# Kernel optimization log

Hardware: AMD Instinct MI355X
Metric: run time of the kernel (lower is better)

The kernel has to match this reference:

```python
import jax, jax.numpy as jnp
import numpy as np
from jax import lax

D_MODEL, D_INNER, D_STATE, D_CONV, DT_RANK = 1024, 2048, 16, 4, 64
B, L = 1, 2048


def setup_inputs() -> dict:
    key = jax.random.key(0)
    ks = jax.random.split(key, 10)
    s = lambda d: 1.0 / np.sqrt(d)
    return {
        "x": jax.random.normal(ks[0], (B, L, D_MODEL), jnp.float32),
        "W_in": jax.random.normal(ks[1], (D_MODEL, 2 * D_INNER), jnp.float32) * s(D_MODEL),
        "conv_w": jax.random.normal(ks[2], (D_INNER, D_CONV), jnp.float32) * s(D_CONV),
        "conv_b": jax.random.normal(ks[3], (D_INNER,), jnp.float32) * 0.01,
        "W_x": jax.random.normal(ks[4], (D_INNER, DT_RANK + 2 * D_STATE), jnp.float32) * s(D_INNER),
        "W_dt": jax.random.normal(ks[5], (DT_RANK, D_INNER), jnp.float32) * s(DT_RANK),
        "b_dt": jax.random.normal(ks[6], (D_INNER,), jnp.float32) * 0.01,
        # A = arange(1, d_state+1) repeated over d_inner; A_log = log(A)
        "A_log": jnp.log(jnp.tile(jnp.arange(1.0, D_STATE + 1.0, dtype=jnp.float32), (D_INNER, 1))),
        "D": jnp.ones((D_INNER,), jnp.float32),
        "W_out": jax.random.normal(ks[7], (D_INNER, D_MODEL), jnp.float32) * s(D_INNER),
    }


def reference(x, W_in, conv_w, conv_b, W_x, W_dt, b_dt, A_log, D, W_out):
    b, l, dm = x.shape
    di, n = A_log.shape[0], A_log.shape[1]
    # input projection + split into conv branch and gate residual
    x_and_res = x @ W_in                          # (b, l, 2*di)
    xc, res = x_and_res[..., :di], x_and_res[..., di:]
    # causal depthwise conv1d (left pad k-1, matches torch padding=k-1 + slice[:l])
    k = conv_w.shape[1]
    xp = jnp.pad(xc, ((0, 0), (k - 1, 0), (0, 0)))
    xconv = conv_b
    for j in range(k):
        xconv = xconv + xp[:, j:j + l, :] * conv_w[:, j]
    xs = jax.nn.silu(xconv)                       # (b, l, di)
    # selection parameters
    x_dbl = xs @ W_x                              # (b, l, dt_rank + 2n)
    dt_r = x_dbl[..., :DT_RANK]
    Bm = x_dbl[..., DT_RANK:DT_RANK + n]          # (b, l, n)
    Cm = x_dbl[..., DT_RANK + n:]                 # (b, l, n)
    dt = jax.nn.softplus(dt_r @ W_dt + b_dt)      # (b, l, di)
    A = -jnp.exp(A_log)                           # (di, n)
    # discretize
    dA = jnp.exp(jnp.einsum('bld,dn->bldn', dt, A))
    dBx = jnp.einsum('bld,bln->bldn', dt, Bm) * xs[..., None]
    # sequential state scan over time
    def step(h, inp):
        dA_t, dBx_t, C_t = inp                    # (b,di,n),(b,di,n),(b,n)
        h = dA_t * h + dBx_t
        y = jnp.einsum('bdn,bn->bd', h, C_t)
        return h, y
    h0 = jnp.zeros((b, di, n), x.dtype)
    hT, ys = lax.scan(step, h0, (dA.transpose(1, 0, 2, 3),
                                 dBx.transpose(1, 0, 2, 3),
                                 Cm.transpose(1, 0, 2)))
    y = ys.transpose(1, 0, 2) + xs * D            # (b, l, di)
    y = y * jax.nn.silu(res)
    out = y @ W_out                               # (b, l, d_model)
    return out, hT
```

## Files before the change

### kernel.cpp

```cpp
#include <hip/hip_runtime.h>
#include <math.h>

#define DM 1024
#define DI 2048
#define NS 16
#define DTR 64
#define LL 2048
#define NXDBL 96
#define NCHUNK 128
#define CHLEN 16

typedef unsigned short u16;
typedef __attribute__((ext_vector_type(8))) short short8;
typedef __attribute__((ext_vector_type(8))) unsigned short us8;
typedef __attribute__((ext_vector_type(4))) float f32x4;

__device__ __forceinline__ float sigmoidf_(float x) { return 1.f / (1.f + __expf(-x)); }
__device__ __forceinline__ float siluf_(float x) { return x * sigmoidf_(x); }
__device__ __forceinline__ float softplus_fast(float x) {
    return fmaxf(x, 0.f) + __logf(1.f + __expf(-fabsf(x)));
}
__device__ __forceinline__ u16 f2b(float f) {
    unsigned u = __float_as_uint(f);
    return (u16)((u + 0x7FFFu + ((u >> 16) & 1u)) >> 16);
}
__device__ __forceinline__ float b2f(u16 h) {
    return __uint_as_float(((unsigned)h) << 16);
}
__device__ __forceinline__ unsigned pack2(float lo, float hi) {
    return (unsigned)f2b(lo) | ((unsigned)f2b(hi) << 16);
}

__device__ __forceinline__ void convT_dev(const float* __restrict__ src,
                                          u16* __restrict__ dst, int R, int C,
                                          int bflat, int gridx, float (*t)[33]) {
    const int tx = threadIdx.x & 31, ty = threadIdx.x >> 5;
    const int c0 = (bflat % gridx) * 32, r0 = (bflat / gridx) * 32;
#pragma unroll
    for (int i = 0; i < 4; i++)
        t[ty + i * 8][tx] = src[(size_t)(r0 + ty + i * 8) * C + c0 + tx];
    __syncthreads();
#pragma unroll
    for (int i = 0; i < 4; i++)
        dst[(size_t)(c0 + ty + i * 8) * R + r0 + tx] = f2b(t[tx][ty + i * 8]);
}

#define PREP_BLOCKS 8640
__global__ __launch_bounds__(256) void prep_all(const float* __restrict__ x,
                                                u16* __restrict__ xb,
                                                const float* __restrict__ W_in,
                                                u16* __restrict__ W_inT,
                                                const float* __restrict__ W_out,
                                                u16* __restrict__ W_outT,
                                                const float* __restrict__ W_x,
                                                u16* __restrict__ W_xT_pad) {
    __shared__ float t[32][33];
    const int b = blockIdx.x;
    if (b < 2048) {
        const int i = (b * 256 + threadIdx.x) * 4;
        float4 v = *(const float4*)&x[i];
        u16 o[4] = {f2b(v.x), f2b(v.y), f2b(v.z), f2b(v.w)};
        *(ushort4*)&xb[i] = *(ushort4*)o;
    } else if (b < 6144) {
        convT_dev(W_in, W_inT, DM, 2 * DI, b - 2048, 2 * DI / 32, t);
    } else if (b < 8192) {
        convT_dev(W_out, W_outT, DI, DM, b - 6144, DM / 32, t);
    } else if (b < 8384) {
        convT_dev(W_x, W_xT_pad, DI, NXDBL, b - 8192, NXDBL / 32, t);
    } else {
        const int i = (b - 8384) * 256 + threadIdx.x;
        if (i < 32 * DI) W_xT_pad[96 * DI + i] = 0;
    }
}

#define WAITV(N) asm volatile("s_waitcnt vmcnt(" #N ")" ::: "memory")
template <int EPI, int NSTEPS>
__global__ __launch_bounds__(256) void gemm_mfma(const u16* __restrict__ A,
                                                 const u16* __restrict__ Bt,
                                                 void* __restrict__ C0,
                                                 void* __restrict__ C1,
                                                 int M, int N, int lda, int nreal) {
    __shared__ u16 As[3][128 * 32];
    __shared__ u16 Bs[3][128 * 32];
    const int tid = threadIdx.x;
    const int lane = tid & 63;
    const int wave = tid >> 6;
    const int gx = gridDim.x, gy = gridDim.y;
    const int nb = gx * gy;
    const int h = blockIdx.y * gx + blockIdx.x;
    const int f = (h & 7) * (nb >> 3) + (h >> 3);
    const int bm = (f % gy) * 128, bn = (f / gy) * 128;
    const int wr = wave >> 1, wc = wave & 1;
    const int k_off = blockIdx.z * (NSTEPS * 32);

    f32x4 acc[4][4];
#pragma unroll
    for (int m = 0; m < 4; m++)
#pragma unroll
        for (int n = 0; n < 4; n++) acc[m][n] = (f32x4)0.f;

    const int srow = tid >> 2;
    const int swz = (tid >> 3) & 3;
    const int skel = (((tid & 3) ^ swz) << 3);
    const u16* Ag0 = A + (size_t)(bm + srow) * lda + k_off + skel;
    const u16* Ag1 = A + (size_t)(bm + 64 + srow) * lda + k_off + skel;
    const u16* Bg0 = Bt + (size_t)(bn + srow) * lda + k_off + skel;
    const u16* Bg1 = Bt + (size_t)(bn + 64 + srow) * lda + k_off + skel;
    u16* Asl = &As[0][0] + tid * 8;
    u16* Bsl = &Bs[0][0] + tid * 8;

    const int rsw = (lane >> 1) & 3;
    const int arow = (wr * 64 + (lane & 15)) * 32 + (((lane >> 4) ^ rsw) << 3);
    const int brow = (wc * 64 + (lane & 15)) * 32 + (((lane >> 4) ^ rsw) << 3);

#define STAGE(buf, ks)                                                               \
    do {                                                                             \
        __builtin_amdgcn_global_load_lds(                                            \
            (const __attribute__((address_space(1))) unsigned*)(Ag0 + (ks)),         \
            (__attribute__((address_space(3))) unsigned*)(Asl + (buf) * 4096),       \
            16, 0, 0);                                                               \
        __builtin_amdgcn_global_load_lds(                                            \
            (const __attribute__((address_space(1))) unsigned*)(Ag1 + (ks)),         \
            (__attribute__((address_space(3))) unsigned*)(Asl + (buf) * 4096 + 2048),\
            16, 0, 0);                                                               \
        __builtin_amdgcn_global_load_lds(                                            \
            (const __attribute__((address_space(1))) unsigned*)(Bg0 + (ks)),         \
            (__attribute__((address_space(3))) unsigned*)(Bsl + (buf) * 4096),       \
            16, 0, 0);                                                               \
        __builtin_amdgcn_global_load_lds(                                            \
            (const __attribute__((address_space(1))) unsigned*)(Bg1 + (ks)),         \
            (__attribute__((address_space(3))) unsigned*)(Bsl + (buf) * 4096 + 2048),\
            16, 0, 0);                                                               \
    } while (0)

#define COMPUTE(buf)                                                                 \
    do {                                                                             \
        short8 av[4], bv[4];                                                         \
        _Pragma("unroll") for (int m = 0; m < 4; m++)                                \
            av[m] = *(const short8*)&As[buf][arow + m * 512];                        \
        _Pragma("unroll") for (int n = 0; n < 4; n++)                                \
            bv[n] = *(const short8*)&Bs[buf][brow + n * 512];                        \
        _Pragma("unroll") for (int m = 0; m < 4; m++)                                \
            _Pragma("unroll") for (int n = 0; n < 4; n++)                            \
                acc[m][n] = __builtin_amdgcn_mfma_f32_16x16x32_bf16(av[m], bv[n],    \
                                                                    acc[m][n], 0, 0, 0); \
    } while (0)

    STAGE(0, 0);
    if (NSTEPS > 1) STAGE(1, 32);
#pragma unroll
    for (int s = 0; s < NSTEPS; ++s) {
        if (s + 2 < NSTEPS) {
            STAGE((s + 2) % 3, (s + 2) * 32);
            WAITV(8);
        } else if (s + 1 < NSTEPS) {
            WAITV(4);
        } else {
            WAITV(0);
        }
        __builtin_amdgcn_s_barrier();
        COMPUTE(s % 3);
        __builtin_amdgcn_s_barrier();
    }
#undef STAGE
#undef COMPUTE

    const int crow0 = bm + wr * 64 + (lane >> 4) * 4;
    const int ccol0 = bn + wc * 64 + (lane & 15);
#pragma unroll
    for (int m = 0; m < 4; m++)
#pragma unroll
        for (int n = 0; n < 4; n++) {
            const int col = ccol0 + n * 16;
#pragma unroll
            for (int r = 0; r < 4; r++) {
                const int row = crow0 + m * 16 + r;
                const float v = acc[m][n][r];
                if (EPI == 1) {
                    if (col < DI)
                        ((u16*)C0)[(size_t)row * DI + col] = f2b(v);
                    else
                        ((u16*)C1)[(size_t)row * DI + col - DI] = f2b(siluf_(v));
                } else if (EPI == 2) {
                    u16* C0z = (u16*)C0 + (size_t)blockIdx.z * M * nreal;
                    if (col < nreal) C0z[(size_t)row * nreal + col] = f2b(v);
                } else {
                    float* C0z = (float*)C0 + (size_t)blockIdx.z * M * nreal;
                    if (col < nreal) C0z[(size_t)row * nreal + col] = v;
                }
            }
        }
}

__global__ __launch_bounds__(256) void gemm128_dt(const float* __restrict__ A,
                                                  const float* __restrict__ B,
                                                  const float* __restrict__ bias,
                                                  const u16* __restrict__ xsb,
                                                  unsigned* __restrict__ dtxs,
                                                  int N, int K, int lda) {
    __shared__ float As[16][132];
    __shared__ float Bs[16][132];
    const int tid = threadIdx.x;
    const int bm = blockIdx.y * 128, bn = blockIdx.x * 128;
    const int ty = tid >> 4, tx = tid & 15;
    float acc[8][8];
#pragma unroll
    for (int i = 0; i < 8; i++)
#pragma unroll
        for (int j = 0; j < 8; j++) acc[i][j] = 0.f;

    const int ar = tid >> 2, ak = (tid & 3) << 2;
    const int bk = tid >> 5, bc = (tid & 31) << 2;

    for (int k0 = 0; k0 < K; k0 += 16) {
        float4 a0 = *(const float4*)&A[(size_t)(bm + ar) * lda + k0 + ak];
        float4 a1 = *(const float4*)&A[(size_t)(bm + ar + 64) * lda + k0 + ak];
        float4 b0 = *(const float4*)&B[(size_t)(k0 + bk) * N + bn + bc];
        float4 b1 = *(const float4*)&B[(size_t)(k0 + bk + 8) * N + bn + bc];
        __syncthreads();
        As[ak + 0][ar] = a0.x; As[ak + 1][ar] = a0.y;
        As[ak + 2][ar] = a0.z; As[ak + 3][ar] = a0.w;
        As[ak + 0][ar + 64] = a1.x; As[ak + 1][ar + 64] = a1.y;
        As[ak + 2][ar + 64] = a1.z; As[ak + 3][ar + 64] = a1.w;
        *(float4*)&Bs[bk][bc] = b0;
        *(float4*)&Bs[bk + 8][bc] = b1;
        __syncthreads();
#pragma unroll
        for (int k = 0; k < 16; k++) {
            float a[8], b[8];
            *(float4*)&a[0] = *(const float4*)&As[k][ty * 8];
            *(float4*)&a[4] = *(const float4*)&As[k][ty * 8 + 4];
            *(float4*)&b[0] = *(const float4*)&Bs[k][tx * 8];
            *(float4*)&b[4] = *(const float4*)&Bs[k][tx * 8 + 4];
#pragma unroll
            for (int i = 0; i < 8; i++)
#pragma unroll
                for (int j = 0; j < 8; j++) acc[i][j] = fmaf(a[i], b[j], acc[i][j]);
        }
    }
#pragma unroll
    for (int i = 0; i < 8; i++) {
        const int row = bm + ty * 8 + i;
#pragma unroll
        for (int j = 0; j < 8; j += 4) {
            const int col = bn + tx * 8 + j;
            const float4 bi = *(const float4*)&bias[col];
            ushort4 xv = *(const ushort4*)&xsb[(size_t)row * N + col];
            unsigned o[4];
            o[0] = (unsigned)f2b(softplus_fast(acc[i][j + 0] + bi.x)) |
                   ((unsigned)xv.x << 16);
            o[1] = (unsigned)f2b(softplus_fast(acc[i][j + 1] + bi.y)) |
                   ((unsigned)xv.y << 16);
            o[2] = (unsigned)f2b(softplus_fast(acc[i][j + 2] + bi.z)) |
                   ((unsigned)xv.z << 16);
            o[3] = (unsigned)f2b(softplus_fast(acc[i][j + 3] + bi.w)) |
                   ((unsigned)xv.w << 16);
            *(uint4*)&dtxs[(size_t)row * N + col] = *(uint4*)o;
        }
    }
}

__global__ __launch_bounds__(256) void sum4b(const u16* __restrict__ p,
                                             float* __restrict__ out, int n) {
    const int i = (blockIdx.x * 256 + threadIdx.x) * 8;
    us8 a = *(const us8*)&p[i];
    us8 b = *(const us8*)&p[(size_t)n + i];
    us8 c = *(const us8*)&p[2 * (size_t)n + i];
    us8 d = *(const us8*)&p[3 * (size_t)n + i];
    float o[8];
#pragma unroll
    for (int q = 0; q < 8; q++)
        o[q] = (b2f(a[q]) + b2f(b[q])) + (b2f(c[q]) + b2f(d[q]));
    *(float4*)&out[i] = *(float4*)&o[0];
    *(float4*)&out[i + 4] = *(float4*)&o[4];
}

__global__ __launch_bounds__(256) void g2reduce(const float* __restrict__ part,
                                                float* __restrict__ xdbl) {
    const int gid = blockIdx.x * 256 + threadIdx.x;
    if (gid < LL * NXDBL) {
        float s = 0.f;
#pragma unroll
        for (int z = 0; z < 16; z++) s += part[(size_t)z * LL * NXDBL + gid];
        xdbl[gid] = s;
    }
}

__global__ __launch_bounds__(256) void conv_silu(const u16* __restrict__ xcb,
                                                 const float* __restrict__ cw,
                                                 const float* __restrict__ cb,
                                                 u16* __restrict__ xsb) {
    const int gid = (blockIdx.x * 256 + threadIdx.x) * 4;
    const int l = gid >> 11;
    const int d = gid & (DI - 1);
    float acc[4];
    {
        float4 b4 = *(const float4*)&cb[d];
        acc[0] = b4.x; acc[1] = b4.y; acc[2] = b4.z; acc[3] = b4.w;
    }
    float4 w0 = *(const float4*)&cw[(d + 0) * 4];
    float4 w1 = *(const float4*)&cw[(d + 1) * 4];
    float4 w2 = *(const float4*)&cw[(d + 2) * 4];
    float4 w3 = *(const float4*)&cw[(d + 3) * 4];
    const float* wp0 = (const float*)&w0;
    const float* wp1 = (const float*)&w1;
    const float* wp2 = (const float*)&w2;
    const float* wp3 = (const float*)&w3;
#pragma unroll
    for (int j = 0; j < 4; j++) {
        const int li = l + j - 3;
        if (li >= 0) {
            ushort4 v = *(const ushort4*)&xcb[(size_t)li * DI + d];
            acc[0] = fmaf(b2f(v.x), wp0[j], acc[0]);
            acc[1] = fmaf(b2f(v.y), wp1[j], acc[1]);
            acc[2] = fmaf(b2f(v.z), wp2[j], acc[2]);
            acc[3] = fmaf(b2f(v.w), wp3[j], acc[3]);
        }
    }
    u16 ob[4] = {f2b(siluf_(acc[0])), f2b(siluf_(acc[1])),
                 f2b(siluf_(acc[2])), f2b(siluf_(acc[3]))};
    *(ushort4*)&xsb[gid] = *(ushort4*)ob;
}

__global__ __launch_bounds__(256) void scan_phase1(const unsigned* __restrict__ dtxs,
                                                   const float* __restrict__ xdbl,
                                                   const float* __restrict__ A_log,
                                                   u16* __restrict__ chA,
                                                   u16* __restrict__ chB) {
    const int g = blockIdx.x * 256 + threadIdx.x;
    const int d = g & (DI - 1);
    const int c = g >> 11;
    float An2[NS], ap[NS], bc[NS];
    {
        float al[NS];
#pragma unroll
        for (int q = 0; q < 4; q++)
            *(float4*)&al[q * 4] = *(const float4*)&A_log[d * NS + q * 4];
#pragma unroll
        for (int n = 0; n < NS; n++) {
            An2[n] = -__expf(al[n]) * 1.44269504f;
            ap[n] = 1.f;
            bc[n] = 0.f;
        }
    }
    const int l0 = c * CHLEN;
    for (int l = l0; l < l0 + CHLEN; ++l) {
        const unsigned dx2 = dtxs[(size_t)l * DI + d];
        const float dtv = b2f((u16)(dx2 & 0xffff));
        const float xsv = b2f((u16)(dx2 >> 16));
        const float dx = dtv * xsv;
        float bv[NS];
#pragma unroll
        for (int q = 0; q < 4; q++)
            *(float4*)&bv[q * 4] = *(const float4*)&xdbl[(size_t)l * NXDBL + DTR + q * 4];
#pragma unroll
        for (int n = 0; n < NS; n++) {
            const float al = __builtin_amdgcn_exp2f(dtv * An2[n]);
            ap[n] *= al;
            bc[n] = fmaf(al, bc[n], dx * bv[n]);
        }
    }
    const size_t o = ((size_t)c * DI + d) * NS;
    u16 ta[NS], tb[NS];
#pragma unroll
    for (int n = 0; n < NS; n++) { ta[n] = f2b(ap[n]); tb[n] = f2b(bc[n]); }
    *(us8*)&chA[o] = *(us8*)&ta[0];
    *(us8*)&chA[o + 8] = *(us8*)&ta[8];
    *(us8*)&chB[o] = *(us8*)&tb[0];
    *(us8*)&chB[o + 8] = *(us8*)&tb[8];
}

__global__ __launch_bounds__(256) void scan_phase2(u16* __restrict__ chA,
                                                   const u16* __restrict__ chB,
                                                   float* __restrict__ hT_out) {
    const int p = blockIdx.x * 256 + threadIdx.x;
    const size_t base = (size_t)2 * p;
    float h0f = 0.f, h1f = 0.f;
#pragma unroll 16
    for (int c = 0; c < NCHUNK; ++c) {
        const size_t o = (size_t)c * DI * NS + base;
        const unsigned av = *(const unsigned*)&chA[o];
        const unsigned bv = *(const unsigned*)&chB[o];
        *(unsigned*)&chA[o] = pack2(h0f, h1f);
        h0f = fmaf(b2f((u16)(av & 0xffff)), h0f, b2f((u16)(bv & 0xffff)));
        h1f = fmaf(b2f((u16)(av >> 16)), h1f, b2f((u16)(bv >> 16)));
    }
    *(float2*)&hT_out[base] = make_float2(h0f, h1f);
}

__global__ __launch_bounds__(256) void scan_phase3(const unsigned* __restrict__ dtxs,
                                                   const float* __restrict__ xdbl,
                                                   const float* __restrict__ A_log,
                                                   const u16* __restrict__ h0,
                                                   const float* __restrict__ Dw,
                                                   const u16* __restrict__ gate,
                                                   u16* __restrict__ yb) {
    const int g = blockIdx.x * 256 + threadIdx.x;
    const int d = g & (DI - 1);
    const int c = g >> 11;
    float An2[NS], h[NS];
    {
        float al[NS];
#pragma unroll
        for (int q = 0; q < 4; q++)
            *(float4*)&al[q * 4] = *(const float4*)&A_log[d * NS + q * 4];
#pragma unroll
        for (int n = 0; n < NS; n++) An2[n] = -__expf(al[n]) * 1.44269504f;
    }
    {
        const size_t ho = ((size_t)c * DI + d) * NS;
        us8 h0a = *(const us8*)&h0[ho];
        us8 h0b = *(const us8*)&h0[ho + 8];
#pragma unroll
        for (int q = 0; q < 8; q++) {
            h[q] = b2f((u16)h0a[q]);
            h[8 + q] = b2f((u16)h0b[q]);
        }
    }
    const float Dd = Dw[d];
    const int l0 = c * CHLEN;
    for (int l = l0; l < l0 + CHLEN; ++l) {
        const unsigned dx2 = dtxs[(size_t)l * DI + d];
        const float dtv = b2f((u16)(dx2 & 0xffff));
        const float xsv = b2f((u16)(dx2 >> 16));
        const float gv = b2f(gate[(size_t)l * DI + d]);
        const float dx = dtv * xsv;
        float bv[NS], cv[NS];
#pragma unroll
        for (int q = 0; q < 4; q++) {
            *(float4*)&bv[q * 4] = *(const float4*)&xdbl[(size_t)l * NXDBL + DTR + q * 4];
            *(float4*)&cv[q * 4] =
                *(const float4*)&xdbl[(size_t)l * NXDBL + DTR + NS + q * 4];
        }
#pragma unroll
        for (int n = 0; n < NS; n++) {
            const float al = __builtin_amdgcn_exp2f(dtv * An2[n]);
            h[n] = fmaf(al, h[n], dx * bv[n]);
        }
        float y0 = 0.f, y1 = 0.f, y2 = 0.f, y3 = 0.f;
#pragma unroll
        for (int n = 0; n < NS; n += 4) {
            y0 = fmaf(h[n + 0], cv[n + 0], y0);
            y1 = fmaf(h[n + 1], cv[n + 1], y1);
            y2 = fmaf(h[n + 2], cv[n + 2], y2);
            y3 = fmaf(h[n + 3], cv[n + 3], y3);
        }
        const float yv = (((y0 + y1) + (y2 + y3)) + xsv * Dd) * gv;
        yb[(size_t)l * DI + d] = f2b(yv);
    }
}

extern "C" void kernel_launch(void* const* d_in, const int* in_sizes, int n_in,
                              void* d_out, int out_size, void* d_ws, size_t ws_size,
                              hipStream_t stream) {
    const float* x = (const float*)d_in[0];
    const float* W_in = (const float*)d_in[1];
    const float* conv_w = (const float*)d_in[2];
    const float* conv_b = (const float*)d_in[3];
    const float* W_x = (const float*)d_in[4];
    const float* W_dt = (const float*)d_in[5];
    const float* b_dt = (const float*)d_in[6];
    const float* A_log = (const float*)d_in[7];
    const float* Dw = (const float*)d_in[8];
    const float* W_out = (const float*)d_in[9];
    float* out = (float*)d_out;

    float* ws = (float*)d_ws;
    u16*      xcb      = (u16*)ws;
    u16*      gate     = (u16*)(ws + 4194304);
    unsigned* dtxs     = (unsigned*)(ws + 8388608);
    float*    xdbl     = ws + 16777216;
    u16*      chA      = (u16*)(ws + 16973824);
    u16*      chB      = (u16*)(ws + 21168128);
    u16*      xb       = (u16*)(ws + 25362432);
    u16*      W_inT_b  = (u16*)(ws + 26411008);
    u16*      W_outT_b = (u16*)(ws + 28508160);
    u16*      xs_b     = (u16*)(ws + 29556736);
    u16*      W_xT_pad = (u16*)(ws + 31653888);
    float*    g2part   = ws + 31784960;
    u16*      g4part   = (u16*)(ws + 35979264);
    u16*      yb       = (u16*)(ws + 44367872);

    prep_all<<<PREP_BLOCKS, 256, 0, stream>>>(x, xb, W_in, W_inT_b, W_out, W_outT_b,
                                              W_x, W_xT_pad);
    gemm_mfma<1, DM / 32><<<dim3(2 * DI / 128, LL / 128), 256, 0, stream>>>(
        xb, W_inT_b, xcb, gate, LL, 2 * DI, DM, 2 * DI);
    conv_silu<<<(LL * DI) / 1024, 256, 0, stream>>>(xcb, conv_w, conv_b, xs_b);
    gemm_mfma<0, 4><<<dim3(1, LL / 128, 16), 256, 0, stream>>>(
        xs_b, W_xT_pad, g2part, nullptr, LL, 128, DI, NXDBL);
    g2reduce<<<(LL * NXDBL + 255) / 256, 256, 0, stream>>>(g2part, xdbl);
    gemm128_dt<<<dim3(DI / 128, LL / 128), 256, 0, stream>>>(xdbl, W_dt, b_dt, xs_b,
                                                             dtxs, DI, DTR, NXDBL);
    scan_phase1<<<(DI * NCHUNK) / 256, 256, 0, stream>>>(dtxs, xdbl, A_log, chA, chB);
    scan_phase2<<<(DI * NS / 2) / 256, 256, 0, stream>>>(chA, chB,
                                                         out + (size_t)LL * DM);
    scan_phase3<<<(DI * NCHUNK) / 256, 256, 0, stream>>>(dtxs, xdbl, A_log, chA, Dw,
                                                         gate, yb);
    gemm_mfma<2, DI / 128><<<dim3(DM / 128, LL / 128, 4), 256, 0, stream>>>(
        yb, W_outT_b, g4part, nullptr, LL, DM, DI, DM);
    sum4b<<<(LL * DM) / 2048, 256, 0, stream>>>(g4part, out, LL * DM);
}
```

Measured before the change: 164.7 us.

## Split chunk-carry scan into two-level super-chunk scan and widen conv_silu vectors

The serial 128-step carry scan across chunks (phase2, only 64 blocks) becomes two levels. A parallel pass composes 8 sub-chunks per super-chunk and writes exclusive local prefixes back into chA/chB. A short 16-step pass then propagates carries across super-chunks, and phase3 rebuilds each chunk's start state from the super-carry plus the local prefix. The aim is to cut the long dependent latency chain and raise parallelism, at the cost of an extra launch and more memory traffic. conv_silu also processes 8 channels per thread with 16-byte loads and stores instead of 4.

```diff
diff --git a/kernel.cpp b/kernel.cpp
--- a/kernel.cpp
+++ b/kernel.cpp
@@ -9,6 +9,8 @@
 #define NXDBL 96
 #define NCHUNK 128
 #define CHLEN 16
+#define NSUPER 16
+#define SUBCH 8
 
 typedef unsigned short u16;
 typedef __attribute__((ext_vector_type(8))) short short8;
@@ -290,36 +292,36 @@
                                                  const float* __restrict__ cw,
                                                  const float* __restrict__ cb,
                                                  u16* __restrict__ xsb) {
-    const int gid = (blockIdx.x * 256 + threadIdx.x) * 4;
+    const int gid = (blockIdx.x * 256 + threadIdx.x) * 8;
     const int l = gid >> 11;
     const int d = gid & (DI - 1);
-    float acc[4];
+    float acc[8];
     {
-        float4 b4 = *(const float4*)&cb[d];
-        acc[0] = b4.x; acc[1] = b4.y; acc[2] = b4.z; acc[3] = b4.w;
-    }
-    float4 w0 = *(const float4*)&cw[(d + 0) * 4];
-    float4 w1 = *(const float4*)&cw[(d + 1) * 4];
-    float4 w2 = *(const float4*)&cw[(d + 2) * 4];
-    float4 w3 = *(const float4*)&cw[(d + 3) * 4];
-    const float* wp0 = (const float*)&w0;
-    const float* wp1 = (const float*)&w1;
-    const float* wp2 = (const float*)&w2;
-    const float* wp3 = (const float*)&w3;
+        float4 b0 = *(const float4*)&cb[d];
+        float4 b1 = *(const float4*)&cb[d + 4];
+        acc[0] = b0.x; acc[1] = b0.y; acc[2] = b0.z; acc[3] = b0.w;
+        acc[4] = b1.x; acc[5] = b1.y; acc[6] = b1.z; acc[7] = b1.w;
+    }
+    float4 w[8];
+#pragma unroll
+    for (int q = 0; q < 8; q++) w[q] = *(const float4*)&cw[(d + q) * 4];
 #pragma unroll
     for (int j = 0; j < 4; j++) {
         const int li = l + j - 3;
         if (li >= 0) {
-            ushort4 v = *(const ushort4*)&xcb[(size_t)li * DI + d];
-            acc[0] = fmaf(b2f(v.x), wp0[j], acc[0]);
-            acc[1] = fmaf(b2f(v.y), wp1[j], acc[1]);
-            acc[2] = fmaf(b2f(v.z), wp2[j], acc[2]);
-            acc[3] = fmaf(b2f(v.w), wp3[j], acc[3]);
-        }
-    }
-    u16 ob[4] = {f2b(siluf_(acc[0])), f2b(siluf_(acc[1])),
-                 f2b(siluf_(acc[2])), f2b(siluf_(acc[3]))};
-    *(ushort4*)&xsb[gid] = *(ushort4*)ob;
+            us8 v = *(const us8*)&xcb[(size_t)li * DI + d];
+            const float wj0[8] = {((const float*)&w[0])[j], ((const float*)&w[1])[j],
+                                  ((const float*)&w[2])[j], ((const float*)&w[3])[j],
+                                  ((const float*)&w[4])[j], ((const float*)&w[5])[j],
+                                  ((const float*)&w[6])[j], ((const float*)&w[7])[j]};
+#pragma unroll
+            for (int q = 0; q < 8; q++) acc[q] = fmaf(b2f(v[q]), wj0[q], acc[q]);
+        }
+    }
+    u16 ob[8];
+#pragma unroll
+    for (int q = 0; q < 8; q++) ob[q] = f2b(siluf_(acc[q]));
+    *(us8*)&xsb[gid] = *(us8*)ob;
 }
 
 __global__ __launch_bounds__(256) void scan_phase1(const unsigned* __restrict__ dtxs,
@@ -370,20 +372,48 @@
     *(us8*)&chB[o + 8] = *(us8*)&tb[8];
 }
 
-__global__ __launch_bounds__(256) void scan_phase2(u16* __restrict__ chA,
-                                                   const u16* __restrict__ chB,
-                                                   float* __restrict__ hT_out) {
+__global__ __launch_bounds__(256) void scan_phase2a(u16* __restrict__ chA,
+                                                    u16* __restrict__ chB,
+                                                    float* __restrict__ supA,
+                                                    float* __restrict__ supB) {
+    const int G = blockIdx.x * 256 + threadIdx.x;
+    const int s = G >> 14;
+    const int p = G & 16383;
+    const size_t base = (size_t)2 * p;
+    float af0 = 1.f, bf0 = 0.f, af1 = 1.f, bf1 = 0.f;
+#pragma unroll
+    for (int k = 0; k < SUBCH; ++k) {
+        const int c = s * SUBCH + k;
+        const size_t o = (size_t)c * DI * NS + base;
+        const unsigned av = *(const unsigned*)&chA[o];
+        const unsigned bvv = *(const unsigned*)&chB[o];
+        *(unsigned*)&chA[o] = pack2(af0, af1);
+        *(unsigned*)&chB[o] = pack2(bf0, bf1);
+        const float a0 = b2f((u16)(av & 0xffff)), a1 = b2f((u16)(av >> 16));
+        const float b0 = b2f((u16)(bvv & 0xffff)), b1 = b2f((u16)(bvv >> 16));
+        bf0 = fmaf(a0, bf0, b0); af0 *= a0;
+        bf1 = fmaf(a1, bf1, b1); af1 *= a1;
+    }
+    const size_t so = (size_t)s * (DI * NS) + base;
+    *(float2*)&supA[so] = make_float2(af0, af1);
+    *(float2*)&supB[so] = make_float2(bf0, bf1);
+}
+
+__global__ __launch_bounds__(256) void scan_phase2b(const float* __restrict__ supA,
+                                                    const float* __restrict__ supB,
+                                                    float* __restrict__ supH,
+                                                    float* __restrict__ hT_out) {
     const int p = blockIdx.x * 256 + threadIdx.x;
     const size_t base = (size_t)2 * p;
     float h0f = 0.f, h1f = 0.f;
-#pragma unroll 16
-    for (int c = 0; c < NCHUNK; ++c) {
-        const size_t o = (size_t)c * DI * NS + base;
-        const unsigned av = *(const unsigned*)&chA[o];
-        const unsigned bv = *(const unsigned*)&chB[o];
-        *(unsigned*)&chA[o] = pack2(h0f, h1f);
-        h0f = fmaf(b2f((u16)(av & 0xffff)), h0f, b2f((u16)(bv & 0xffff)));
-        h1f = fmaf(b2f((u16)(av >> 16)), h1f, b2f((u16)(bv >> 16)));
+#pragma unroll
+    for (int s = 0; s < NSUPER; ++s) {
+        const size_t o = (size_t)s * (DI * NS) + base;
+        const float2 a = *(const float2*)&supA[o];
+        const float2 b = *(const float2*)&supB[o];
+        *(float2*)&supH[o] = make_float2(h0f, h1f);
+        h0f = fmaf(a.x, h0f, b.x);
+        h1f = fmaf(a.y, h1f, b.y);
     }
     *(float2*)&hT_out[base] = make_float2(h0f, h1f);
 }
@@ -391,13 +421,16 @@
 __global__ __launch_bounds__(256) void scan_phase3(const unsigned* __restrict__ dtxs,
                                                    const float* __restrict__ xdbl,
                                                    const float* __restrict__ A_log,
-                                                   const u16* __restrict__ h0,
+                                                   const u16* __restrict__ chA,
+                                                   const u16* __restrict__ chB,
+                                                   const float* __restrict__ supH,
                                                    const float* __restrict__ Dw,
                                                    const u16* __restrict__ gate,
                                                    u16* __restrict__ yb) {
     const int g = blockIdx.x * 256 + threadIdx.x;
     const int d = g & (DI - 1);
     const int c = g >> 11;
+    const int s = c >> 3;
     float An2[NS], h[NS];
     {
         float al[NS];
@@ -409,12 +442,19 @@
     }
     {
         const size_t ho = ((size_t)c * DI + d) * NS;
-        us8 h0a = *(const us8*)&h0[ho];
-        us8 h0b = *(const us8*)&h0[ho + 8];
+        const size_t so = ((size_t)s * DI + d) * NS;
+        us8 ap0 = *(const us8*)&chA[ho];
+        us8 ap1 = *(const us8*)&chA[ho + 8];
+        us8 bp0 = *(const us8*)&chB[ho];
+        us8 bp1 = *(const us8*)&chB[ho + 8];
+        float sh[NS];
+#pragma unroll
+        for (int q = 0; q < 4; q++)
+            *(float4*)&sh[q * 4] = *(const float4*)&supH[so + q * 4];
 #pragma unroll
         for (int q = 0; q < 8; q++) {
-            h[q] = b2f((u16)h0a[q]);
-            h[8 + q] = b2f((u16)h0b[q]);
+            h[q] = fmaf(b2f((u16)ap0[q]), sh[q], b2f((u16)bp0[q]));
+            h[8 + q] = fmaf(b2f((u16)ap1[q]), sh[8 + q], b2f((u16)bp1[q]));
         }
     }
     const float Dd = Dw[d];
@@ -480,22 +520,27 @@
     float*    g2part   = ws + 31784960;
     u16*      g4part   = (u16*)(ws + 35979264);
     u16*      yb       = (u16*)(ws + 44367872);
+    float*    supA     = ws + 46465024;
+    float*    supB     = ws + 46989312;
+    float*    supH     = ws + 47513600;
 
     prep_all<<<PREP_BLOCKS, 256, 0, stream>>>(x, xb, W_in, W_inT_b, W_out, W_outT_b,
                                               W_x, W_xT_pad);
     gemm_mfma<1, DM / 32><<<dim3(2 * DI / 128, LL / 128), 256, 0, stream>>>(
         xb, W_inT_b, xcb, gate, LL, 2 * DI, DM, 2 * DI);
-    conv_silu<<<(LL * DI) / 1024, 256, 0, stream>>>(xcb, conv_w, conv_b, xs_b);
+    conv_silu<<<(LL * DI) / 2048, 256, 0, stream>>>(xcb, conv_w, conv_b, xs_b);
     gemm_mfma<0, 4><<<dim3(1, LL / 128, 16), 256, 0, stream>>>(
         xs_b, W_xT_pad, g2part, nullptr, LL, 128, DI, NXDBL);
     g2reduce<<<(LL * NXDBL + 255) / 256, 256, 0, stream>>>(g2part, xdbl);
     gemm128_dt<<<dim3(DI / 128, LL / 128), 256, 0, stream>>>(xdbl, W_dt, b_dt, xs_b,
                                                              dtxs, DI, DTR, NXDBL);
     scan_phase1<<<(DI * NCHUNK) / 256, 256, 0, stream>>>(dtxs, xdbl, A_log, chA, chB);
-    scan_phase2<<<(DI * NS / 2) / 256, 256, 0, stream>>>(chA, chB,
-                                                         out + (size_t)LL * DM);
-    scan_phase3<<<(DI * NCHUNK) / 256, 256, 0, stream>>>(dtxs, xdbl, A_log, chA, Dw,
-                                                         gate, yb);
+    scan_phase2a<<<(NSUPER * DI * NS / 2) / 256, 256, 0, stream>>>(chA, chB, supA,
+                                                                   supB);
+    scan_phase2b<<<(DI * NS / 2) / 256, 256, 0, stream>>>(supA, supB, supH,
+                                                          out + (size_t)LL * DM);
+    scan_phase3<<<(DI * NCHUNK) / 256, 256, 0, stream>>>(dtxs, xdbl, A_log, chA, chB,
+                                                         supH, Dw, gate, yb);
     gemm_mfma<2, DI / 128><<<dim3(DM / 128, LL / 128, 4), 256, 0, stream>>>(
         yb, W_outT_b, g4part, nullptr, LL, DM, DI, DM);
     sum4b<<<(LL * DM) / 2048, 256, 0, stream>>>(g4part, out, LL * DM);
```

Measured after the change: 168.8 us. +2.4%, slower.
